# Kernel optimization log

Measured on AMD Instinct MI355X. Metric: run time of the kernel, lower is better.

## Reference

```python
import jax, jax.numpy as jnp
import numpy as np

WH, WW = 7, 7
SH, SW = 3, 3
NUM_HEADS = 8


def _rel_pos_index(wh, ww):
    coords = np.stack(np.meshgrid(np.arange(wh), np.arange(ww), indexing='ij')).reshape(2, -1)
    rel = (coords[:, :, None] - coords[:, None, :]).transpose(1, 2, 0)  # [N,N,2]
    rel[..., 0] += wh - 1
    rel[..., 1] += ww - 1
    rel[..., 0] *= 2 * ww - 1
    return rel.sum(-1)  # [N,N] int


def _attn_mask(Hp, Wp, wh, ww, sh, sw):
    img = np.zeros((Hp, Wp), dtype=np.float32)
    cnt = 0
    for hs in (slice(0, -wh), slice(-wh, -sh), slice(-sh, None)):
        for ws in (slice(0, -ww), slice(-ww, -sw), slice(-sw, None)):
            img[hs, ws] = cnt
            cnt += 1
    win = img.reshape(Hp // wh, wh, Wp // ww, ww).transpose(0, 2, 1, 3).reshape(-1, wh * ww)  # [nW,N]
    diff = win[:, None, :] - win[:, :, None]  # [nW,N,N]
    return np.where(diff != 0, -100.0, 0.0).astype(np.float32)


def _layernorm(x, g, b, eps=1e-5):
    mu = jnp.mean(x, -1, keepdims=True)
    var = jnp.mean(jnp.square(x - mu), -1, keepdims=True)
    return (x - mu) * jax.lax.rsqrt(var + eps) * g + b


def setup_inputs() -> dict:
    key = jax.random.key(0)
    ks = jax.random.split(key, 12)
    B, H, W, C = 32, 56, 56, 256
    hid = 4 * C
    s = lambda k, *shape: jax.random.normal(k, shape, jnp.float32) * 0.02
    return {
        'x': jax.random.normal(ks[0], (B, H * W, C), jnp.float32),
        'g1': jnp.ones((C,), jnp.float32), 'b1': jnp.zeros((C,), jnp.float32),
        'qkv_w': s(ks[1], 3 * C, C), 'qkv_b': jnp.zeros((3 * C,), jnp.float32),
        'bias_table': s(ks[2], (2 * WH - 1) * (2 * WW - 1), NUM_HEADS),
        'proj_w': s(ks[3], C, C), 'proj_b': jnp.zeros((C,), jnp.float32),
        'g2': jnp.ones((C,), jnp.float32), 'b2': jnp.zeros((C,), jnp.float32),
        'w1': s(ks[4], hid, C), 'bm1': jnp.zeros((hid,), jnp.float32),
        'w2': s(ks[5], C, hid), 'bm2': jnp.zeros((C,), jnp.float32),
        'H': H, 'W': W,
    }


def reference(x, g1, b1, qkv_w, qkv_b, bias_table, proj_w, proj_b, g2, b2, w1, bm1, w2, bm2, H, W):
    B, L, C = x.shape
    wh, ww = WH, WW
    nH = NUM_HEADS
    hd = C // nH
    scale = hd ** -0.5
    N = wh * ww

    shortcut = x
    h = _layernorm(x, g1, b1).reshape(B, H, W, C)
    pad_b = (wh - H % wh) % wh
    pad_r = (ww - W % ww) % ww
    if pad_b or pad_r:
        h = jnp.pad(h, ((0, 0), (0, pad_b), (0, pad_r), (0, 0)))
    Hp, Wp = h.shape[1], h.shape[2]

    h = jnp.roll(h, (-SH, -SW), axis=(1, 2))
    # window partition -> [B*nW, N, C]
    nWh, nWw = Hp // wh, Wp // ww
    xw = h.reshape(B, nWh, wh, nWw, ww, C).transpose(0, 1, 3, 2, 4, 5).reshape(-1, N, C)

    qkv = jnp.einsum('bnc,oc->bno', xw, qkv_w) + qkv_b  # [B*nW, N, 3C]
    qkv = qkv.reshape(-1, N, 3, nH, hd).transpose(2, 0, 3, 1, 4)
    q, k, v = qkv[0] * scale, qkv[1], qkv[2]  # [B*nW, nH, N, hd]
    attn = jnp.einsum('whnd,whmd->whnm', q, k)  # [B*nW, nH, N, N]

    rpi = jnp.asarray(_rel_pos_index(wh, ww))
    bias = bias_table[rpi.reshape(-1)].reshape(N, N, nH).transpose(2, 0, 1)  # [nH,N,N]
    attn = attn + bias[None]

    mask = jnp.asarray(_attn_mask(Hp, Wp, wh, ww, SH, SW))  # [nW,N,N]
    nW = mask.shape[0]
    attn = attn.reshape(B, nW, nH, N, N) + mask[None, :, None]
    attn = jax.nn.softmax(attn.reshape(-1, nH, N, N), axis=-1)

    out = jnp.einsum('whnm,whmd->whnd', attn, v).transpose(0, 2, 1, 3).reshape(-1, N, C)
    out = jnp.einsum('bnc,oc->bno', out, proj_w) + proj_b

    # window reverse
    out = out.reshape(B, nWh, nWw, wh, ww, C).transpose(0, 1, 3, 2, 4, 5).reshape(B, Hp, Wp, C)
    out = jnp.roll(out, (SH, SW), axis=(1, 2))
    if pad_b or pad_r:
        out = out[:, :H, :W, :]
    out = out.reshape(B, H * W, C)

    x = shortcut + out
    m = _layernorm(x, g2, b2)
    m = jax.nn.gelu(jnp.einsum('blc,oc->blo', m, w1) + bm1, approximate=False)
    m = jnp.einsum('blh,oh->blo', m, w2) + bm2
    return x + m
```

## Files before the change

kernel.cpp:

```cpp
#include <hip/hip_runtime.h>
#include <hip/hip_bf16.h>

#define DEVI __device__ __forceinline__
#define AS1 __attribute__((address_space(1)))
#define AS3 __attribute__((address_space(3)))

typedef short bf16x8 __attribute__((ext_vector_type(8)));
typedef float f32x4  __attribute__((ext_vector_type(4)));
typedef unsigned short u16x4 __attribute__((ext_vector_type(4)));

constexpr int MROWS = 100352;

DEVI int win_row_to_token(int r) {
  int b   = r / 3136;
  int rem = r - b * 3136;
  int wi  = rem / 49;
  int t   = rem - wi * 49;
  int nwh = wi >> 3, nww = wi & 7;
  int th = t / 7, tw = t - th * 7;
  int h = nwh * 7 + th + 3; if (h >= 56) h -= 56;
  int w = nww * 7 + tw + 3; if (w >= 56) w -= 56;
  return b * 3136 + h * 56 + w;
}

DEVI unsigned short f2bf(float f) {
  __hip_bfloat16 h = __float2bfloat16(f);
  return __builtin_bit_cast(unsigned short, h);
}

__global__ void cvt_kernel(const float* __restrict__ in, __hip_bfloat16* __restrict__ out, int n) {
  int i = blockIdx.x * 256 + threadIdx.x;
  if (i < n) out[i] = __float2bfloat16(in[i]);
}

template<bool WIN>
__global__ __launch_bounds__(256) void ln_kernel(
    const float* __restrict__ xin, const float* __restrict__ g,
    const float* __restrict__ b, __hip_bfloat16* __restrict__ outb)
{
  int r = blockIdx.x * 4 + (threadIdx.x >> 6);
  int l = threadIdx.x & 63;
  int tok = WIN ? win_row_to_token(r) : r;
  float4 xv = *(const float4*)&xin[(size_t)tok * 256 + l * 4];
  float s = xv.x + xv.y + xv.z + xv.w;
  float q = xv.x * xv.x + xv.y * xv.y + xv.z * xv.z + xv.w * xv.w;
  #pragma unroll
  for (int off = 32; off; off >>= 1) { s += __shfl_xor(s, off); q += __shfl_xor(q, off); }
  float mu = s * (1.0f / 256.0f);
  float var = q * (1.0f / 256.0f) - mu * mu;
  float rs = rsqrtf(var + 1e-5f);
  float4 gv = *(const float4*)&g[l * 4];
  float4 bv = *(const float4*)&b[l * 4];
  ushort4 st;
  st.x = f2bf((xv.x - mu) * rs * gv.x + bv.x);
  st.y = f2bf((xv.y - mu) * rs * gv.y + bv.y);
  st.z = f2bf((xv.z - mu) * rs * gv.z + bv.z);
  st.w = f2bf((xv.w - mu) * rs * gv.w + bv.w);
  *(ushort4*)&outb[(size_t)r * 256 + l * 4] = st;
}

enum { EPI_QKV = 0, EPI_PROJ = 1, EPI_MLP1 = 2, EPI_MLP2 = 3 };

template<int EPI, int KTOT>
__global__ __launch_bounds__(256) void strip5(
    const __hip_bfloat16* __restrict__ A,
    const __hip_bfloat16* __restrict__ Bw,
    int ntiles,
    const float* __restrict__ bias,
    const float* __restrict__ xres,
    float* __restrict__ outf,
    __hip_bfloat16* __restrict__ outb)
{
  constexpr int NKB = KTOT / 256;
  constexpr int NCH = NKB * 4;
  constexpr int K2  = KTOT * 2;
  constexpr long TSTRIDE = 128L * K2;
  __shared__ __align__(16) __hip_bfloat16 Bl[128 * 256];
  __shared__ __align__(16) __hip_bfloat16 Al[128 * 64];

  const int tid = threadIdx.x;
  const int w = tid >> 6, l = tid & 63;
  const int wr = w >> 1, wc = w & 1;
  const int g = l >> 4, lm = l & 15;

  const int xcd = blockIdx.x & 7;
  const int cu2 = blockIdx.x >> 3;
  const int T   = 98 * ntiles;
  const int t0  = (cu2 * T) >> 6;
  const int t1  = ((cu2 + 1) * T) >> 6;

  char* AlB = (char*)Al;
  char* BlB = (char*)Bl;

  const int  dstW = w * 1024;
  const long aoff = (long)(tid >> 3) * K2 + (((tid & 7) ^ ((tid >> 3) & 7)) << 4);
  const long boff = (long)(tid >> 5) * K2 + (((tid & 31) ^ ((tid >> 5) & 7)) << 4);
  const int  bA = (wr * 64 + lm) * 128 + ((g ^ (lm & 7)) << 4);
  const int  bB = (wc * 64 + lm) * 512 + ((g ^ (lm & 7)) << 4);

  int nt = t0 / 98;
  int mtoff = t0 - nt * 98;
  const char* Ab = (const char*)A + (long)xcd * 98 * TSTRIDE;
  const char* At = Ab + (long)mtoff * TSTRIDE;

  auto issueA = [&](const char* Atile, int ch) {
    #pragma unroll
    for (int j = 0; j < 4; ++j)
      __builtin_amdgcn_global_load_lds(
          (const AS1 void*)(Atile + aoff + j * (32L * K2) + ch * 128),
          (AS3 void*)(AlB + j * 4096 + dstW), 16, 0, 0);
  };
  auto stageB = [&](int nt_, int kb_) {
    const char* Bb = (const char*)Bw + (long)nt_ * 128 * K2 + kb_ * 512;
    #pragma unroll
    for (int j = 0; j < 16; ++j)
      __builtin_amdgcn_global_load_lds(
          (const AS1 void*)(Bb + boff + j * (8L * K2)),
          (AS3 void*)(BlB + j * 4096 + dstW), 16, 0, 0);
  };

  stageB(nt, 0);
  issueA(At, 0);

  f32x4 acc[4][4];
  for (int t = t0; t < t1; ++t) {
    const bool wrap = (mtoff == 97);
    const char* Atn = wrap ? Ab : (At + TSTRIDE);
    const int ntn = wrap ? nt + 1 : nt;
    const int colb = nt * 128 + wc * 64 + g * 4;

    f32x4 bias_v[4];
    #pragma unroll
    for (int ni = 0; ni < 4; ++ni)
      bias_v[ni] = *(const f32x4*)&bias[colb + ni * 16];
    #pragma unroll
    for (int mi = 0; mi < 4; ++mi)
      #pragma unroll
      for (int ni = 0; ni < 4; ++ni)
        acc[mi][ni] = bias_v[ni];

    #pragma unroll
    for (int kb = 0; kb < NKB; ++kb) {
      #pragma unroll
      for (int c4 = 0; c4 < 4; ++c4) {
        const int ch = kb * 4 + c4;
        asm volatile("s_waitcnt vmcnt(0)" ::: "memory");
        __builtin_amdgcn_s_barrier();
        asm volatile("" ::: "memory");

        #pragma unroll
        for (int kk = 0; kk < 2; ++kk) {
          bf16x8 af[4], bf[4];
          const int ax = bA ^ (kk << 6);
          const int bx = bB ^ (kk << 6);
          #pragma unroll
          for (int mi = 0; mi < 4; ++mi)
            af[mi] = *(const bf16x8*)(AlB + ax + mi * 2048);
          #pragma unroll
          for (int ni = 0; ni < 4; ++ni)
            bf[ni] = *(const bf16x8*)(BlB + bx + c4 * 128 + ni * 8192);
          #pragma unroll
          for (int mi = 0; mi < 4; ++mi)
            #pragma unroll
            for (int ni = 0; ni < 4; ++ni)
              acc[mi][ni] = __builtin_amdgcn_mfma_f32_16x16x32_bf16(
                  bf[ni], af[mi], acc[mi][ni], 0, 0, 0);
        }

        asm volatile("" ::: "memory");
        __builtin_amdgcn_s_barrier();
        if (ch < NCH - 1) {
          if (NKB > 1 && c4 == 3) stageB(nt, kb + 1);
          issueA(At, ch + 1);
        } else if (t < t1 - 1) {
          if (NKB > 1) stageB(ntn, 0);
          else if (ntn != nt) stageB(ntn, 0);
          issueA(Atn, 0);
        }
      }
    }

    {
      const int mt = xcd * 98 + mtoff;
      #pragma unroll
      for (int mi = 0; mi < 4; ++mi) {
        int grow = mt * 128 + wr * 64 + mi * 16 + lm;
        if (EPI == EPI_QKV) {
          __hip_bfloat16* rp = outb + (size_t)grow * 768 + colb;
          #pragma unroll
          for (int ni = 0; ni < 4; ++ni) {
            u16x4 st = { f2bf(acc[mi][ni][0]), f2bf(acc[mi][ni][1]),
                         f2bf(acc[mi][ni][2]), f2bf(acc[mi][ni][3]) };
            *(u16x4*)(rp + ni * 16) = st;
          }
        } else if (EPI == EPI_PROJ) {
          int orow = win_row_to_token(grow);
          const f32x4* xr = (const f32x4*)(xres + (size_t)orow * 256 + colb);
          f32x4* op = (f32x4*)(outf + (size_t)orow * 256 + colb);
          #pragma unroll
          for (int ni = 0; ni < 4; ++ni)
            op[ni * 4] = xr[ni * 4] + acc[mi][ni];
        } else if (EPI == EPI_MLP1) {
          __hip_bfloat16* rp = outb + (size_t)grow * 1024 + colb;
          #pragma unroll
          for (int ni = 0; ni < 4; ++ni) {
            u16x4 st;
            #pragma unroll
            for (int j = 0; j < 4; ++j) {
              float v = acc[mi][ni][j];
              float u2 = v * (1.5957691216f + 0.1426930877f * v * v);
              float e  = __expf(u2);
              st[j] = f2bf(v * e / (e + 1.0f));
            }
            *(u16x4*)(rp + ni * 16) = st;
          }
        } else {
          f32x4* op = (f32x4*)(outf + (size_t)grow * 256 + colb);
          #pragma unroll
          for (int ni = 0; ni < 4; ++ni)
            op[ni * 4] = op[ni * 4] + acc[mi][ni];
        }
      }
    }

    At = Atn;
    if (wrap) { mtoff = 0; nt = ntn; } else { ++mtoff; }
  }
}

__global__ __launch_bounds__(256) void bias_prep_kernel(
    const float* __restrict__ bt, float* __restrict__ Sadd)
{
  int blk = blockIdx.x;
  int cls = blk >> 3, h = blk & 7;
  int re = cls >> 1, ce = cls & 1;
  int lane = threadIdx.x & 63, fs = threadIdx.x >> 6;
  int g = lane >> 4, lm = lane & 15;
  #pragma unroll
  for (int i = 0; i < 4; ++i) {
    int f = fs * 4 + i;
    int mi = f >> 2, ni = f & 3;
    int key = ni * 16 + lm;
    f32x4 v;
    #pragma unroll
    for (int j = 0; j < 4; ++j) {
      int q = mi * 16 + g * 4 + j;
      float val;
      if (key >= 49) {
        val = -1e30f;
      } else {
        int qq = q > 48 ? 48 : q;
        int qh = qq / 7, qw = qq - qh * 7;
        int kh = key / 7, kw = key - kh * 7;
        int rpi = (qh - kh + 6) * 13 + (qw - kw + 6);
        val = bt[rpi * 8 + h];
        int rq = (re ? (qh < 4 ? 1 : 2) : 0) * 3 + (ce ? (qw < 4 ? 1 : 2) : 0);
        int rk = (re ? (kh < 4 ? 1 : 2) : 0) * 3 + (ce ? (kw < 4 ? 1 : 2) : 0);
        if (rq != rk) val -= 100.0f;
      }
      v[j] = val;
    }
    ((f32x4*)Sadd)[(blk * 16 + f) * 64 + lane] = v;
  }
}

__global__ __launch_bounds__(256) void attn_mfma_kernel(
    const __hip_bfloat16* __restrict__ qkv,
    const float* __restrict__ Sadd,
    __hip_bfloat16* __restrict__ attn_out)
{
  __shared__ __align__(16) __hip_bfloat16 Pl[4][64 * 72];
  int blk = blockIdx.x;
  int win = blk >> 1, half = blk & 1;
  int w = threadIdx.x >> 6, l = threadIdx.x & 63;
  int head = half * 4 + w;
  int g = l >> 4, lm = l & 15;
  int wi = win & 63;
  int cls = (((wi >> 3) == 7) ? 2 : 0) | (((wi & 7) == 7) ? 1 : 0);
  const __hip_bfloat16* base = qkv + (size_t)win * 49 * 768 + head * 32;

  bf16x8 aQ[4], bK[4];
  #pragma unroll
  for (int mi = 0; mi < 4; ++mi) {
    int q = mi * 16 + lm; if (q > 48) q = 48;
    aQ[mi] = *(const bf16x8*)(base + q * 768 + g * 8);
  }
  #pragma unroll
  for (int ni = 0; ni < 4; ++ni) {
    int k = ni * 16 + lm; if (k > 48) k = 48;
    bK[ni] = *(const bf16x8*)(base + 256 + k * 768 + g * 8);
  }
  f32x4 acc[4][4] = {};
  #pragma unroll
  for (int mi = 0; mi < 4; ++mi)
    #pragma unroll
    for (int ni = 0; ni < 4; ++ni)
      acc[mi][ni] = __builtin_amdgcn_mfma_f32_16x16x32_bf16(aQ[mi], bK[ni], acc[mi][ni], 0, 0, 0);

  const float scale = 0.17677669529663687f;
  const f32x4* Sb = (const f32x4*)Sadd + (size_t)(cls * 8 + head) * 16 * 64 + l;

  f32x4 rsum[4];
  __hip_bfloat16* P = Pl[w];
  #pragma unroll
  for (int mi = 0; mi < 4; ++mi) {
    #pragma unroll
    for (int ni = 0; ni < 4; ++ni) {
      f32x4 sv = Sb[(mi * 4 + ni) * 64];
      #pragma unroll
      for (int j = 0; j < 4; ++j) acc[mi][ni][j] = acc[mi][ni][j] * scale + sv[j];
    }
    f32x4 mx = acc[mi][0];
    #pragma unroll
    for (int ni = 1; ni < 4; ++ni)
      #pragma unroll
      for (int j = 0; j < 4; ++j) mx[j] = fmaxf(mx[j], acc[mi][ni][j]);
    #pragma unroll
    for (int msk = 1; msk < 16; msk <<= 1)
      #pragma unroll
      for (int j = 0; j < 4; ++j) mx[j] = fmaxf(mx[j], __shfl_xor(mx[j], msk));
    f32x4 sm = {};
    #pragma unroll
    for (int ni = 0; ni < 4; ++ni)
      #pragma unroll
      for (int j = 0; j < 4; ++j) {
        float e = __expf(acc[mi][ni][j] - mx[j]);
        acc[mi][ni][j] = e;
        sm[j] += e;
      }
    #pragma unroll
    for (int msk = 1; msk < 16; msk <<= 1)
      #pragma unroll
      for (int j = 0; j < 4; ++j) sm[j] += __shfl_xor(sm[j], msk);
    rsum[mi] = sm;
    #pragma unroll
    for (int ni = 0; ni < 4; ++ni)
      #pragma unroll
      for (int j = 0; j < 4; ++j) {
        int q = mi * 16 + g * 4 + j;
        int key = ni * 16 + lm;
        P[q * 72 + key] = __float2bfloat16(acc[mi][ni][j]);
      }
  }

  bf16x8 bV[2][2];
  #pragma unroll
  for (int s = 0; s < 2; ++s)
    #pragma unroll
    for (int n2 = 0; n2 < 2; ++n2) {
      bf16x8 vv;
      #pragma unroll
      for (int e = 0; e < 8; ++e) {
        int key = s * 32 + g * 8 + e; if (key > 48) key = 48;
        vv[e] = __builtin_bit_cast(short, base[512 + key * 768 + n2 * 16 + lm]);
      }
      bV[s][n2] = vv;
    }

  f32x4 o[4][2] = {};
  #pragma unroll
  for (int s = 0; s < 2; ++s)
    #pragma unroll
    for (int mi2 = 0; mi2 < 4; ++mi2) {
      bf16x8 aP = *(const bf16x8*)&P[(mi2 * 16 + lm) * 72 + s * 32 + g * 8];
      #pragma unroll
      for (int n2 = 0; n2 < 2; ++n2)
        o[mi2][n2] = __builtin_amdgcn_mfma_f32_16x16x32_bf16(aP, bV[s][n2], o[mi2][n2], 0, 0, 0);
    }

  #pragma unroll
  for (int mi2 = 0; mi2 < 4; ++mi2) {
    f32x4 li;
    #pragma unroll
    for (int j = 0; j < 4; ++j) li[j] = 1.0f / rsum[mi2][j];
    #pragma unroll
    for (int n2 = 0; n2 < 2; ++n2)
      #pragma unroll
      for (int j = 0; j < 4; ++j) {
        int q = mi2 * 16 + g * 4 + j;
        if (q < 49)
          attn_out[((size_t)win * 49 + q) * 256 + head * 32 + n2 * 16 + lm] =
              __float2bfloat16(o[mi2][n2][j] * li[j]);
      }
  }
}

extern "C" void kernel_launch(void* const* d_in, const int* in_sizes, int n_in,
                              void* d_out, int out_size, void* d_ws, size_t ws_size,
                              hipStream_t stream) {
  const float* x          = (const float*)d_in[0];
  const float* g1         = (const float*)d_in[1];
  const float* b1         = (const float*)d_in[2];
  const float* qkv_w      = (const float*)d_in[3];
  const float* qkv_b      = (const float*)d_in[4];
  const float* bias_table = (const float*)d_in[5];
  const float* proj_w     = (const float*)d_in[6];
  const float* proj_b     = (const float*)d_in[7];
  const float* g2         = (const float*)d_in[8];
  const float* b2         = (const float*)d_in[9];
  const float* w1         = (const float*)d_in[10];
  const float* bm1        = (const float*)d_in[11];
  const float* w2         = (const float*)d_in[12];
  const float* bm2        = (const float*)d_in[13];
  float* out = (float*)d_out;

  char* ws = (char*)d_ws;
  __hip_bfloat16* A_ln   = (__hip_bfloat16*)(ws);
  __hip_bfloat16* qkvb   = (__hip_bfloat16*)(ws + 51380224);
  __hip_bfloat16* attn_o = (__hip_bfloat16*)(ws + 205520896);
  __hip_bfloat16* hidden = qkvb;
  __hip_bfloat16* qkv_wb  = (__hip_bfloat16*)(ws + 256901120);
  __hip_bfloat16* proj_wb = qkv_wb + 196608;
  __hip_bfloat16* w1b     = proj_wb + 65536;
  __hip_bfloat16* w2b     = w1b + 262144;
  float* Sadd = (float*)(ws + 258473984);

  cvt_kernel<<<(196608 + 255) / 256, 256, 0, stream>>>(qkv_w, qkv_wb, 196608);
  cvt_kernel<<<(65536  + 255) / 256, 256, 0, stream>>>(proj_w, proj_wb, 65536);
  cvt_kernel<<<(262144 + 255) / 256, 256, 0, stream>>>(w1, w1b, 262144);
  cvt_kernel<<<(262144 + 255) / 256, 256, 0, stream>>>(w2, w2b, 262144);
  bias_prep_kernel<<<32, 256, 0, stream>>>(bias_table, Sadd);

  ln_kernel<true><<<MROWS / 4, 256, 0, stream>>>(x, g1, b1, A_ln);

  strip5<EPI_QKV, 256><<<512, 256, 0, stream>>>(
      A_ln, qkv_wb, 6, qkv_b, nullptr, nullptr, qkvb);

  attn_mfma_kernel<<<4096, 256, 0, stream>>>(qkvb, Sadd, attn_o);

  strip5<EPI_PROJ, 256><<<512, 256, 0, stream>>>(
      attn_o, proj_wb, 2, proj_b, x, out, nullptr);

  ln_kernel<false><<<MROWS / 4, 256, 0, stream>>>(out, g2, b2, A_ln);

  strip5<EPI_MLP1, 256><<<512, 256, 0, stream>>>(
      A_ln, w1b, 8, bm1, nullptr, nullptr, hidden);

  strip5<EPI_MLP2, 1024><<<512, 256, 0, stream>>>(
      hidden, w2b, 2, bm2, nullptr, out, nullptr);
}
```

Before: 523.4 us.

## Replace persistent strip GEMM with single-wavefront 128x64 tile GEMM kernels

Replaces the persistent 256-thread strip GEMM with a one-wave-per-block kernel. Each block computes one 128x64 output tile, so the launch covers the full tile grid instead of a fixed set of persistent blocks. A tiles stream into a 4-slot LDS ring via global_load_lds, B fragments are loaded straight into registers with double buffering, and partial vmcnt waits replace block barriers. It adds an XCD-aware block swizzle. In exchange it loses B reuse from LDS across waves and makes many more small blocks, each with 128 accumulator registers.

```diff
diff --git a/kernel.cpp b/kernel.cpp
--- a/kernel.cpp
+++ b/kernel.cpp
@@ -62,169 +62,130 @@
 enum { EPI_QKV = 0, EPI_PROJ = 1, EPI_MLP1 = 2, EPI_MLP2 = 3 };
 
 template<int EPI, int KTOT>
-__global__ __launch_bounds__(256) void strip5(
+__global__ __launch_bounds__(64, 2) void gemm64(
     const __hip_bfloat16* __restrict__ A,
     const __hip_bfloat16* __restrict__ Bw,
-    int ntiles,
+    int ntn,
     const float* __restrict__ bias,
     const float* __restrict__ xres,
     float* __restrict__ outf,
     __hip_bfloat16* __restrict__ outb)
 {
-  constexpr int NKB = KTOT / 256;
-  constexpr int NCH = NKB * 4;
+  constexpr int NCH = KTOT / 32;
   constexpr int K2  = KTOT * 2;
-  constexpr long TSTRIDE = 128L * K2;
-  __shared__ __align__(16) __hip_bfloat16 Bl[128 * 256];
-  __shared__ __align__(16) __hip_bfloat16 Al[128 * 64];
-
-  const int tid = threadIdx.x;
-  const int w = tid >> 6, l = tid & 63;
-  const int wr = w >> 1, wc = w & 1;
+  __shared__ __align__(16) __hip_bfloat16 Al[4][128 * 32];
+
+  const int l = threadIdx.x;
   const int g = l >> 4, lm = l & 15;
 
-  const int xcd = blockIdx.x & 7;
-  const int cu2 = blockIdx.x >> 3;
-  const int T   = 98 * ntiles;
-  const int t0  = (cu2 * T) >> 6;
-  const int t1  = ((cu2 + 1) * T) >> 6;
-
+  const int nwg = gridDim.x;
+  int bswz = (blockIdx.x & 7) * (nwg >> 3) + (blockIdx.x >> 3);
+  const int mt = bswz / ntn;
+  const int nt = bswz - mt * ntn;
+
+  const char* At = (const char*)A + (size_t)mt * 128 * K2;
+  const char* Bt = (const char*)Bw + ((size_t)nt * 64 + lm) * K2 + (g << 4);
+
+  long asrc[8];
+  #pragma unroll
+  for (int j = 0; j < 8; ++j) {
+    int U = j * 64 + l;
+    int row = U >> 2, u = U & 3;
+    asrc[j] = (long)row * K2 + ((u ^ ((row >> 1) & 3)) << 4);
+  }
   char* AlB = (char*)Al;
-  char* BlB = (char*)Bl;
-
-  const int  dstW = w * 1024;
-  const long aoff = (long)(tid >> 3) * K2 + (((tid & 7) ^ ((tid >> 3) & 7)) << 4);
-  const long boff = (long)(tid >> 5) * K2 + (((tid & 31) ^ ((tid >> 5) & 7)) << 4);
-  const int  bA = (wr * 64 + lm) * 128 + ((g ^ (lm & 7)) << 4);
-  const int  bB = (wc * 64 + lm) * 512 + ((g ^ (lm & 7)) << 4);
-
-  int nt = t0 / 98;
-  int mtoff = t0 - nt * 98;
-  const char* Ab = (const char*)A + (long)xcd * 98 * TSTRIDE;
-  const char* At = Ab + (long)mtoff * TSTRIDE;
-
-  auto issueA = [&](const char* Atile, int ch) {
-    #pragma unroll
-    for (int j = 0; j < 4; ++j)
+  const int aoff = lm * 64 + ((g ^ ((lm >> 1) & 3)) << 4);
+
+  const int colb = nt * 64 + g * 4;
+  f32x4 acc[8][4];
+  {
+    f32x4 bias_v[4];
+    #pragma unroll
+    for (int ni = 0; ni < 4; ++ni) bias_v[ni] = *(const f32x4*)&bias[colb + ni * 16];
+    #pragma unroll
+    for (int mi = 0; mi < 8; ++mi)
+      #pragma unroll
+      for (int ni = 0; ni < 4; ++ni) acc[mi][ni] = bias_v[ni];
+  }
+
+  bf16x8 bf[2][4];
+  auto issueA = [&](int ch, int slot) {
+    #pragma unroll
+    for (int j = 0; j < 8; ++j)
       __builtin_amdgcn_global_load_lds(
-          (const AS1 void*)(Atile + aoff + j * (32L * K2) + ch * 128),
-          (AS3 void*)(AlB + j * 4096 + dstW), 16, 0, 0);
+          (const AS1 void*)(At + asrc[j] + ch * 64),
+          (AS3 void*)(AlB + slot * 8192 + j * 1024), 16, 0, 0);
   };
-  auto stageB = [&](int nt_, int kb_) {
-    const char* Bb = (const char*)Bw + (long)nt_ * 128 * K2 + kb_ * 512;
-    #pragma unroll
-    for (int j = 0; j < 16; ++j)
-      __builtin_amdgcn_global_load_lds(
-          (const AS1 void*)(Bb + boff + j * (8L * K2)),
-          (AS3 void*)(BlB + j * 4096 + dstW), 16, 0, 0);
+  auto loadB = [&](int ch, int s) {
+    #pragma unroll
+    for (int ni = 0; ni < 4; ++ni)
+      bf[s][ni] = *(const bf16x8*)(Bt + (long)ni * 16 * K2 + ch * 64);
   };
 
-  stageB(nt, 0);
-  issueA(At, 0);
-
-  f32x4 acc[4][4];
-  for (int t = t0; t < t1; ++t) {
-    const bool wrap = (mtoff == 97);
-    const char* Atn = wrap ? Ab : (At + TSTRIDE);
-    const int ntn = wrap ? nt + 1 : nt;
-    const int colb = nt * 128 + wc * 64 + g * 4;
-
-    f32x4 bias_v[4];
-    #pragma unroll
-    for (int ni = 0; ni < 4; ++ni)
-      bias_v[ni] = *(const f32x4*)&bias[colb + ni * 16];
-    #pragma unroll
-    for (int mi = 0; mi < 4; ++mi)
+  issueA(0, 0); loadB(0, 0);
+  asm volatile("" ::: "memory");
+  issueA(1, 1); loadB(1, 1);
+
+  #pragma unroll
+  for (int i = 0; i < NCH; ++i) {
+    if (i < NCH - 1) {
+      asm volatile("s_waitcnt vmcnt(12)" ::: "memory");
+    } else {
+      asm volatile("s_waitcnt vmcnt(0)" ::: "memory");
+    }
+    const char* bb = AlB + (i & 3) * 8192;
+    #pragma unroll
+    for (int mi = 0; mi < 8; ++mi) {
+      bf16x8 af = *(const bf16x8*)(bb + mi * 1024 + aoff);
       #pragma unroll
       for (int ni = 0; ni < 4; ++ni)
-        acc[mi][ni] = bias_v[ni];
-
-    #pragma unroll
-    for (int kb = 0; kb < NKB; ++kb) {
-      #pragma unroll
-      for (int c4 = 0; c4 < 4; ++c4) {
-        const int ch = kb * 4 + c4;
-        asm volatile("s_waitcnt vmcnt(0)" ::: "memory");
-        __builtin_amdgcn_s_barrier();
-        asm volatile("" ::: "memory");
-
+        acc[mi][ni] = __builtin_amdgcn_mfma_f32_16x16x32_bf16(
+            bf[i & 1][ni], af, acc[mi][ni], 0, 0, 0);
+    }
+    if (i < NCH - 2) {
+      issueA(i + 2, (i + 2) & 3);
+      loadB(i + 2, i & 1);
+    }
+  }
+
+  #pragma unroll
+  for (int mi = 0; mi < 8; ++mi) {
+    int grow = mt * 128 + mi * 16 + lm;
+    if (EPI == EPI_QKV) {
+      __hip_bfloat16* rp = outb + (size_t)grow * 768 + colb;
+      #pragma unroll
+      for (int ni = 0; ni < 4; ++ni) {
+        u16x4 st = { f2bf(acc[mi][ni][0]), f2bf(acc[mi][ni][1]),
+                     f2bf(acc[mi][ni][2]), f2bf(acc[mi][ni][3]) };
+        *(u16x4*)(rp + ni * 16) = st;
+      }
+    } else if (EPI == EPI_PROJ) {
+      int orow = win_row_to_token(grow);
+      const f32x4* xr = (const f32x4*)(xres + (size_t)orow * 256 + colb);
+      f32x4* op = (f32x4*)(outf + (size_t)orow * 256 + colb);
+      #pragma unroll
+      for (int ni = 0; ni < 4; ++ni)
+        op[ni * 4] = xr[ni * 4] + acc[mi][ni];
+    } else if (EPI == EPI_MLP1) {
+      __hip_bfloat16* rp = outb + (size_t)grow * 1024 + colb;
+      #pragma unroll
+      for (int ni = 0; ni < 4; ++ni) {
+        u16x4 st;
         #pragma unroll
-        for (int kk = 0; kk < 2; ++kk) {
-          bf16x8 af[4], bf[4];
-          const int ax = bA ^ (kk << 6);
-          const int bx = bB ^ (kk << 6);
-          #pragma unroll
-          for (int mi = 0; mi < 4; ++mi)
-            af[mi] = *(const bf16x8*)(AlB + ax + mi * 2048);
-          #pragma unroll
-          for (int ni = 0; ni < 4; ++ni)
-            bf[ni] = *(const bf16x8*)(BlB + bx + c4 * 128 + ni * 8192);
-          #pragma unroll
-          for (int mi = 0; mi < 4; ++mi)
-            #pragma unroll
-            for (int ni = 0; ni < 4; ++ni)
-              acc[mi][ni] = __builtin_amdgcn_mfma_f32_16x16x32_bf16(
-                  bf[ni], af[mi], acc[mi][ni], 0, 0, 0);
+        for (int j = 0; j < 4; ++j) {
+          float v = acc[mi][ni][j];
+          float u2 = v * (1.5957691216f + 0.1426930877f * v * v);
+          float e  = __expf(u2);
+          st[j] = f2bf(v * e / (e + 1.0f));
         }
-
-        asm volatile("" ::: "memory");
-        __builtin_amdgcn_s_barrier();
-        if (ch < NCH - 1) {
-          if (NKB > 1 && c4 == 3) stageB(nt, kb + 1);
-          issueA(At, ch + 1);
-        } else if (t < t1 - 1) {
-          if (NKB > 1) stageB(ntn, 0);
-          else if (ntn != nt) stageB(ntn, 0);
-          issueA(Atn, 0);
-        }
-      }
-    }
-
-    {
-      const int mt = xcd * 98 + mtoff;
-      #pragma unroll
-      for (int mi = 0; mi < 4; ++mi) {
-        int grow = mt * 128 + wr * 64 + mi * 16 + lm;
-        if (EPI == EPI_QKV) {
-          __hip_bfloat16* rp = outb + (size_t)grow * 768 + colb;
-          #pragma unroll
-          for (int ni = 0; ni < 4; ++ni) {
-            u16x4 st = { f2bf(acc[mi][ni][0]), f2bf(acc[mi][ni][1]),
-                         f2bf(acc[mi][ni][2]), f2bf(acc[mi][ni][3]) };
-            *(u16x4*)(rp + ni * 16) = st;
-          }
-        } else if (EPI == EPI_PROJ) {
-          int orow = win_row_to_token(grow);
-          const f32x4* xr = (const f32x4*)(xres + (size_t)orow * 256 + colb);
-          f32x4* op = (f32x4*)(outf + (size_t)orow * 256 + colb);
-          #pragma unroll
-          for (int ni = 0; ni < 4; ++ni)
-            op[ni * 4] = xr[ni * 4] + acc[mi][ni];
-        } else if (EPI == EPI_MLP1) {
-          __hip_bfloat16* rp = outb + (size_t)grow * 1024 + colb;
-          #pragma unroll
-          for (int ni = 0; ni < 4; ++ni) {
-            u16x4 st;
-            #pragma unroll
-            for (int j = 0; j < 4; ++j) {
-              float v = acc[mi][ni][j];
-              float u2 = v * (1.5957691216f + 0.1426930877f * v * v);
-              float e  = __expf(u2);
-              st[j] = f2bf(v * e / (e + 1.0f));
-            }
-            *(u16x4*)(rp + ni * 16) = st;
-          }
-        } else {
-          f32x4* op = (f32x4*)(outf + (size_t)grow * 256 + colb);
-          #pragma unroll
-          for (int ni = 0; ni < 4; ++ni)
-            op[ni * 4] = op[ni * 4] + acc[mi][ni];
-        }
-      }
-    }
-
-    At = Atn;
-    if (wrap) { mtoff = 0; nt = ntn; } else { ++mtoff; }
+        *(u16x4*)(rp + ni * 16) = st;
+      }
+    } else {
+      f32x4* op = (f32x4*)(outf + (size_t)grow * 256 + colb);
+      #pragma unroll
+      for (int ni = 0; ni < 4; ++ni)
+        op[ni * 4] = op[ni * 4] + acc[mi][ni];
+    }
   }
 }
 
@@ -423,19 +384,19 @@
 
   ln_kernel<true><<<MROWS / 4, 256, 0, stream>>>(x, g1, b1, A_ln);
 
-  strip5<EPI_QKV, 256><<<512, 256, 0, stream>>>(
-      A_ln, qkv_wb, 6, qkv_b, nullptr, nullptr, qkvb);
+  gemm64<EPI_QKV, 256><<<784 * 12, 64, 0, stream>>>(
+      A_ln, qkv_wb, 12, qkv_b, nullptr, nullptr, qkvb);
 
   attn_mfma_kernel<<<4096, 256, 0, stream>>>(qkvb, Sadd, attn_o);
 
-  strip5<EPI_PROJ, 256><<<512, 256, 0, stream>>>(
-      attn_o, proj_wb, 2, proj_b, x, out, nullptr);
+  gemm64<EPI_PROJ, 256><<<784 * 4, 64, 0, stream>>>(
+      attn_o, proj_wb, 4, proj_b, x, out, nullptr);
 
   ln_kernel<false><<<MROWS / 4, 256, 0, stream>>>(out, g2, b2, A_ln);
 
-  strip5<EPI_MLP1, 256><<<512, 256, 0, stream>>>(
-      A_ln, w1b, 8, bm1, nullptr, nullptr, hidden);
-
-  strip5<EPI_MLP2, 1024><<<512, 256, 0, stream>>>(
-      hidden, w2b, 2, bm2, nullptr, out, nullptr);
-}
+  gemm64<EPI_MLP1, 256><<<784 * 16, 64, 0, stream>>>(
+      A_ln, w1b, 16, bm1, nullptr, nullptr, hidden);
+
+  gemm64<EPI_MLP2, 1024><<<784 * 4, 64, 0, stream>>>(
+      hidden, w2b, 4, bm2, nullptr, out, nullptr);
+}
```

Result: slower. 603.9 us (+15.4%).
